# Optimization experiments

Measured on AMD Instinct MI355X. Metric: run time of the kernel, lower is better.

## Reference

```python
import jax, jax.numpy as jnp
import numpy as np

ODIM = 8192      # output dim (slice target)
MSIZE = 64       # tile size
N_BLOCKS = 1024  # size of shared block bank


def setup_inputs() -> dict:
    key = jax.random.key(0)
    k1, k2, k3, k4 = jax.random.split(key, 4)
    x = jax.random.normal(k1, (256, 8192), dtype=jnp.float32)
    # bank of msize x msize module blocks (scaled like fan-in init)
    blocks = jax.random.normal(k2, (N_BLOCKS, MSIZE, MSIZE), dtype=jnp.float32) * 0.02
    bound = 1.0 / np.sqrt(ODIM).astype(np.float32)
    bias = jax.random.uniform(k3, (ODIM,), dtype=jnp.float32, minval=-bound, maxval=bound)
    # parts: [icount, ocount] indices into the block bank
    parts = jax.random.randint(k4, (128, 128), 0, N_BLOCKS)
    return {"x": x, "blocks": blocks, "bias": bias, "parts": parts}


def reference(x, blocks, bias, parts):
    icount, ocount = parts.shape
    m = blocks.shape[-1]
    # build_mosaic: gather blocks per parts and tile into a dense weight matrix
    fc = blocks[parts]                                   # [ic, oc, m, m]
    fc_mat = fc.transpose(0, 2, 1, 3).reshape(icount * m, ocount * m)
    # idim (8192) is divisible by msize, so pad is identity (rem == 0 branch)
    y = x @ fc_mat                                       # [B, oc*m]
    y = y[..., :ODIM] + bias                             # slice + bias; post = Identity
    return y
```

## Files before the change

### kernel.cpp

```cpp
#include <hip/hip_runtime.h>
#include <stdint.h>

#define BATCH 256
#define IDIM  8192
#define ODIM  8192
#define MS    64
#define IC    128
#define OC    128
#define NB    1024

#define BM 256
#define BN 256
#define BK 64
#define KSPLIT 8
#define KT (IC / KSPLIT)

#define ABUF(s) ((s) * 16384)
#define BBUF(s) (32768 + (s) * 16384)

typedef __bf16 bf16x8 __attribute__((ext_vector_type(8)));
typedef float  floatx4 __attribute__((ext_vector_type(4)));

#define WAITCNT_VM(n) ((((n) & 15) | (((n) >> 4) << 14)) | 0x70 | 0xF00)

__device__ __forceinline__ void async_load16(unsigned short* lds_p, const unsigned short* g_p) {
    __builtin_amdgcn_global_load_lds(
        (const __attribute__((address_space(1))) unsigned int*)g_p,
        (__attribute__((address_space(3))) unsigned int*)lds_p,
        16, 0, 0);
}

__device__ __forceinline__ unsigned short f32_to_bf16(float f) {
    unsigned int u = __float_as_uint(f);
    u += 0x7FFFu + ((u >> 16) & 1u);
    return (unsigned short)(u >> 16);
}

#define XCONV_BLKS 1024
#define PT_BLKS 64
__global__ void k_convert(const float* __restrict__ x, const float* __restrict__ blocks,
                          const int* __restrict__ parts,
                          unsigned short* __restrict__ xb, unsigned short* __restrict__ bt,
                          int* __restrict__ pT) {
    __shared__ float tile[MS][MS + 1];
    int b = blockIdx.x;
    if (b < NB) {
        const float4* src4 = (const float4*)(blocks + (size_t)b * MS * MS);
        unsigned short* dst = bt + (size_t)b * MS * MS;
        #pragma unroll
        for (int i = 0; i < 4; ++i) {
            int slot = i * 256 + threadIdx.x;
            int r = slot >> 4, c4 = (slot & 15) * 4;
            float4 v = src4[slot];
            tile[r][c4 + 0] = v.x; tile[r][c4 + 1] = v.y;
            tile[r][c4 + 2] = v.z; tile[r][c4 + 3] = v.w;
        }
        __syncthreads();
        #pragma unroll
        for (int i = 0; i < 2; ++i) {
            int slot = i * 256 + threadIdx.x;
            int c = slot >> 3, o = slot & 7;
            union { unsigned short s[8]; uint4 v; } u;
            #pragma unroll
            for (int j = 0; j < 8; ++j) u.s[j] = f32_to_bf16(tile[o * 8 + j][c]);
            *(uint4*)(dst + c * MS + o * 8) = u.v;
        }
    } else if (b < NB + XCONV_BLKS) {
        int t = (b - NB) * 256 + threadIdx.x;
        const float4* x4 = (const float4*)x;
        float4 a = x4[2 * t], bb = x4[2 * t + 1];
        union { unsigned short s[8]; uint4 v; } u;
        u.s[0] = f32_to_bf16(a.x);  u.s[1] = f32_to_bf16(a.y);
        u.s[2] = f32_to_bf16(a.z);  u.s[3] = f32_to_bf16(a.w);
        u.s[4] = f32_to_bf16(bb.x); u.s[5] = f32_to_bf16(bb.y);
        u.s[6] = f32_to_bf16(bb.z); u.s[7] = f32_to_bf16(bb.w);
        ((uint4*)xb)[t] = u.v;
    } else {
        int t = (b - NB - XCONV_BLKS) * 256 + threadIdx.x;
        int oc = t >> 7, ic = t & 127;
        pT[t] = parts[ic * OC + oc];
    }
}

extern __shared__ unsigned short smem[];

__global__ __launch_bounds__(512, 2)
void k_mosaic_gemm(const unsigned short* __restrict__ xb,
                   const unsigned short* __restrict__ bt,
                   const int* __restrict__ pT,
                   float* __restrict__ partial) {
    const int tid  = threadIdx.x;
    const int lane = tid & 63;
    const int wave = tid >> 6;
    const int wrow = wave >> 2;
    const int wcol = wave & 3;
    const int ks = blockIdx.x;
    const int nt = blockIdx.y;

    const int ob0 = nt * 4;
    const int kb0 = ks * KT;

    const int row  = lane & 15;
    const int quad = lane >> 4;

    int pv = pT[(ob0 + quad) * IC + kb0 + row];

    const int swz0 = ((quad)     ^ (row & 7)) << 3;
    const int swz1 = ((quad + 4) ^ (row & 7)) << 3;
    const int a_b0 = (wrow * 128 + row) * MS + swz0;
    const int a_b1 = (wrow * 128 + row) * MS + swz1;
    const int b_b0 = (wcol * 64 + row) * MS + swz0;
    const int b_b1 = (wcol * 64 + row) * MS + swz1;

    floatx4 acc[8][4];
    #pragma unroll
    for (int mi = 0; mi < 8; ++mi)
        #pragma unroll
        for (int ni = 0; ni < 4; ++ni)
            acc[mi][ni] = (floatx4){0.f, 0.f, 0.f, 0.f};

    bf16x8 af[4], bfr[4];

#define STAGE_A(dstS, kb) do {                                                \
    _Pragma("unroll")                                                         \
    for (int j = 0; j < 4; ++j) {                                             \
        int slot = j * 512 + tid;               \
        int m = slot >> 3;                                                    \
        int oct = (slot & 7) ^ (m & 7);                                       \
        async_load16(smem + ABUF(dstS) + slot * 8,                            \
                     xb + (size_t)m * IDIM + (kb) * MS + oct * 8);            \
    } } while (0)

#define STAGE_B(dstS, tt) do {                                                \
    _Pragma("unroll")                                                         \
    for (int j = 0; j < 4; ++j) {                                             \
        int q = __shfl(pv, j * 16 + (tt));                                    \
        int slot = j * 512 + tid;                                             \
        int n = slot >> 3;                                                    \
        int oct = (slot & 7) ^ (n & 7);                                       \
        async_load16(smem + BBUF(dstS) + slot * 8,                            \
                     bt + (size_t)q * (MS * MS) + (n & 63) * MS + oct * 8);   \
    } } while (0)

#define LOAD_A(S, abase, mh) do {                                             \
    _Pragma("unroll")                                                         \
    for (int mi = 0; mi < 4; ++mi)                                            \
        af[mi] = *(const bf16x8*)(smem + ABUF(S) + (abase) + (mh) * 4096 + mi * 1024); \
    } while (0)

#define LOAD_B(S, bbase) do {                                                 \
    _Pragma("unroll")                                                         \
    for (int ni = 0; ni < 4; ++ni)                                            \
        bfr[ni] = *(const bf16x8*)(smem + BBUF(S) + (bbase) + ni * 1024);     \
    } while (0)

#define MFMA16(mh) do {                                                       \
    _Pragma("unroll")                                                         \
    for (int mi = 0; mi < 4; ++mi)                                            \
        _Pragma("unroll")                                                     \
        for (int ni = 0; ni < 4; ++ni)                                        \
            acc[(mh) * 4 + mi][ni] = __builtin_amdgcn_mfma_f32_16x16x32_bf16( \
                af[mi], bfr[ni], acc[(mh) * 4 + mi][ni], 0, 0, 0);            \
    } while (0)

#define COMPUTE(AS, BS) do {                                                  \
    LOAD_A(AS, a_b0, 0); LOAD_B(BS, b_b0); MFMA16(0);                         \
    LOAD_A(AS, a_b0, 1);                   MFMA16(1);                         \
    LOAD_A(AS, a_b1, 0); LOAD_B(BS, b_b1); MFMA16(0);                         \
    LOAD_A(AS, a_b1, 1);                   MFMA16(1);                         \
    } while (0)

#define TILE(t, AS, BS, AN, BN2, STA, STB, WN) do {                           \
    if (STA) STAGE_A(AN, kb0 + (t) + 1);                                      \
    if (STB) STAGE_B(BN2, (t) + 2);                                           \
    __builtin_amdgcn_sched_barrier(0);                                        \
    __builtin_amdgcn_s_waitcnt(WAITCNT_VM(WN));                               \
    __builtin_amdgcn_s_barrier();                                             \
    __builtin_amdgcn_sched_barrier(0);                                        \
    COMPUTE(AS, BS);                                                          \
    __builtin_amdgcn_sched_barrier(0);                                        \
    __builtin_amdgcn_s_barrier();                                             \
    __builtin_amdgcn_sched_barrier(0);                                        \
    } while (0)

    STAGE_A(0, kb0);
    STAGE_B(0, 0);
    STAGE_B(1, 1);

    #pragma unroll 1
    for (int t6 = 0; t6 < 12; t6 += 6) {
        TILE(t6 + 0, 0, 0, 1, 2, 1, 1, 12);
        TILE(t6 + 1, 1, 1, 0, 0, 1, 1, 12);
        TILE(t6 + 2, 0, 2, 1, 1, 1, 1, 12);
        TILE(t6 + 3, 1, 0, 0, 2, 1, 1, 12);
        TILE(t6 + 4, 0, 1, 1, 0, 1, 1, 12);
        TILE(t6 + 5, 1, 2, 0, 1, 1, 1, 12);
    }
    TILE(12, 0, 0, 1, 2, 1, 1, 12);
    TILE(13, 1, 1, 0, 0, 1, 1, 12);
    TILE(14, 0, 2, 1, 0, 1, 0, 8);
    TILE(15, 1, 0, 0, 0, 0, 0, 0);

    float* out = partial + (size_t)ks * ((size_t)BATCH * ODIM);
    #pragma unroll
    for (int mi8 = 0; mi8 < 8; ++mi8)
        #pragma unroll
        for (int ni = 0; ni < 4; ++ni)
            #pragma unroll
            for (int r = 0; r < 4; ++r) {
                int rowg = wrow * 128 + mi8 * 16 + quad * 4 + r;
                int colg = nt * BN + wcol * 64 + ni * 16 + row;
                out[(size_t)rowg * ODIM + colg] = acc[mi8][ni][r];
            }
}

__global__ void k_reduce_bias(const float* __restrict__ partial,
                              const float* __restrict__ bias,
                              float* __restrict__ out) {
    int t = blockIdx.x * 256 + threadIdx.x;
    const float4* b4 = (const float4*)bias;
    float4 c = b4[t & (ODIM / 4 - 1)];
    float4 r = {c.x, c.y, c.z, c.w};
    #pragma unroll
    for (int k = 0; k < KSPLIT; ++k) {
        const float4* p = (const float4*)(partial + (size_t)k * BATCH * ODIM);
        float4 a = p[t];
        r.x += a.x; r.y += a.y; r.z += a.z; r.w += a.w;
    }
    ((float4*)out)[t] = r;
}

extern "C" void kernel_launch(void* const* d_in, const int* in_sizes, int n_in,
                              void* d_out, int out_size, void* d_ws, size_t ws_size,
                              hipStream_t stream) {
    const float* x      = (const float*)d_in[0];
    const float* blocks = (const float*)d_in[1];
    const float* bias   = (const float*)d_in[2];
    const int*   parts  = (const int*)d_in[3];
    float* out = (float*)d_out;

    char* ws = (char*)d_ws;
    unsigned short* xb      = (unsigned short*)ws;
    unsigned short* btb     = (unsigned short*)(ws + (4u << 20));
    int*            pTr     = (int*)(ws + (12u << 20));
    float*          partial = (float*)(ws + (13u << 20));

    static bool attr_set = false;
    if (!attr_set) {
        hipFuncSetAttribute((const void*)k_mosaic_gemm,
                            hipFuncAttributeMaxDynamicSharedMemorySize, 160 * 1024);
        attr_set = true;
    }

    k_convert<<<NB + XCONV_BLKS + PT_BLKS, 256, 0, stream>>>(x, blocks, parts, xb, btb, pTr);
    k_mosaic_gemm<<<dim3(KSPLIT, ODIM / BN), 512, 160 * 1024, stream>>>(xb, btb, pTr, partial);
    k_reduce_bias<<<(BATCH * ODIM) / (256 * 4), 256, 0, stream>>>(partial, bias, out);
}
```

Baseline: 128.6 us.

## Load B fragments directly from global into registers, drop LDS staging for B

Rather than staging the gathered weight blocks into LDS with async copies, each wave now reads its B fragments straight from global memory into registers. The fragments are double-buffered in two register sets, with the load for the next k-half issued in the middle of the current tile's MFMAs. This removes the B LDS buffers, so the LDS request drops from 160KB to 64KB, and removes LDS read traffic for B. The cost is more global/L2 load latency exposed to the waves, less cross-wave reuse of B, and higher register pressure. The waitcnt counts were also changed, which may not match the new load counts.

Measured after the change: 135.9 us. 1.06x slower.

```diff
diff --git a/kernel.cpp b/kernel.cpp
--- a/kernel.cpp
+++ b/kernel.cpp
@@ -11,12 +11,10 @@
 
 #define BM 256
 #define BN 256
-#define BK 64
 #define KSPLIT 8
 #define KT (IC / KSPLIT)
 
 #define ABUF(s) ((s) * 16384)
-#define BBUF(s) (32768 + (s) * 16384)
 
 typedef __bf16 bf16x8 __attribute__((ext_vector_type(8)));
 typedef float  floatx4 __attribute__((ext_vector_type(4)));
@@ -109,8 +107,8 @@
     const int swz1 = ((quad + 4) ^ (row & 7)) << 3;
     const int a_b0 = (wrow * 128 + row) * MS + swz0;
     const int a_b1 = (wrow * 128 + row) * MS + swz1;
-    const int b_b0 = (wcol * 64 + row) * MS + swz0;
-    const int b_b1 = (wcol * 64 + row) * MS + swz1;
+
+    const int b_off = row * (MS * 2) + quad * 16;
 
     floatx4 acc[8][4];
     #pragma unroll
@@ -119,7 +117,8 @@
         for (int ni = 0; ni < 4; ++ni)
             acc[mi][ni] = (floatx4){0.f, 0.f, 0.f, 0.f};
 
-    bf16x8 af[4], bfr[4];
+    bf16x8 af[4];
+    bf16x8 bk0[4], bk1[4];
 
 #define STAGE_A(dstS, kb) do {                                                \
     _Pragma("unroll")                                                         \
@@ -131,16 +130,14 @@
                      xb + (size_t)m * IDIM + (kb) * MS + oct * 8);            \
     } } while (0)
 
-#define STAGE_B(dstS, tt) do {                                                \
-    _Pragma("unroll")                                                         \
-    for (int j = 0; j < 4; ++j) {                                             \
-        int q = __shfl(pv, j * 16 + (tt));                                    \
-        int slot = j * 512 + tid;                                             \
-        int n = slot >> 3;                                                    \
-        int oct = (slot & 7) ^ (n & 7);                                       \
-        async_load16(smem + BBUF(dstS) + slot * 8,                            \
-                     bt + (size_t)q * (MS * MS) + (n & 63) * MS + oct * 8);   \
-    } } while (0)
+#define LOADB(dstB, tt, kkh) do {                                             \
+    int q = __builtin_amdgcn_readfirstlane(__shfl(pv, wcol * 16 + (tt)));     \
+    const char* bq = (const char*)(bt + (size_t)q * (MS * MS)) + b_off        \
+                     + (kkh) * 64;                                            \
+    _Pragma("unroll")                                                         \
+    for (int ni = 0; ni < 4; ++ni)                                            \
+        dstB[ni] = *(const bf16x8*)(bq + ni * 2048);                          \
+    } while (0)
 
 #define LOAD_A(S, abase, mh) do {                                             \
     _Pragma("unroll")                                                         \
@@ -148,58 +145,44 @@
         af[mi] = *(const bf16x8*)(smem + ABUF(S) + (abase) + (mh) * 4096 + mi * 1024); \
     } while (0)
 
-#define LOAD_B(S, bbase) do {                                                 \
-    _Pragma("unroll")                                                         \
-    for (int ni = 0; ni < 4; ++ni)                                            \
-        bfr[ni] = *(const bf16x8*)(smem + BBUF(S) + (bbase) + ni * 1024);     \
-    } while (0)
-
-#define MFMA16(mh) do {                                                       \
+#define MFMA16(mh, BB) do {                                                   \
     _Pragma("unroll")                                                         \
     for (int mi = 0; mi < 4; ++mi)                                            \
         _Pragma("unroll")                                                     \
         for (int ni = 0; ni < 4; ++ni)                                        \
             acc[(mh) * 4 + mi][ni] = __builtin_amdgcn_mfma_f32_16x16x32_bf16( \
-                af[mi], bfr[ni], acc[(mh) * 4 + mi][ni], 0, 0, 0);            \
-    } while (0)
-
-#define COMPUTE(AS, BS) do {                                                  \
-    LOAD_A(AS, a_b0, 0); LOAD_B(BS, b_b0); MFMA16(0);                         \
-    LOAD_A(AS, a_b0, 1);                   MFMA16(1);                         \
-    LOAD_A(AS, a_b1, 0); LOAD_B(BS, b_b1); MFMA16(0);                         \
-    LOAD_A(AS, a_b1, 1);                   MFMA16(1);                         \
-    } while (0)
-
-#define TILE(t, AS, BS, AN, BN2, STA, STB, WN) do {                           \
+                af[mi], BB[ni], acc[(mh) * 4 + mi][ni], 0, 0, 0);             \
+    } while (0)
+
+#define TILE(t, AS, AN, STA, MIDB, WN) do {                                   \
     if (STA) STAGE_A(AN, kb0 + (t) + 1);                                      \
-    if (STB) STAGE_B(BN2, (t) + 2);                                           \
+    LOADB(bk1, (t), 1);                                                       \
     __builtin_amdgcn_sched_barrier(0);                                        \
     __builtin_amdgcn_s_waitcnt(WAITCNT_VM(WN));                               \
     __builtin_amdgcn_s_barrier();                                             \
     __builtin_amdgcn_sched_barrier(0);                                        \
-    COMPUTE(AS, BS);                                                          \
+    LOAD_A(AS, a_b0, 0); MFMA16(0, bk0);                                      \
+    LOAD_A(AS, a_b0, 1); MFMA16(1, bk0);                                      \
+    __builtin_amdgcn_sched_barrier(0);                                        \
+    if (MIDB) LOADB(bk0, (t) + 1, 0);                                         \
+    __builtin_amdgcn_sched_barrier(0);                                        \
+    LOAD_A(AS, a_b1, 0); MFMA16(0, bk1);                                      \
+    LOAD_A(AS, a_b1, 1); MFMA16(1, bk1);                                      \
     __builtin_amdgcn_sched_barrier(0);                                        \
     __builtin_amdgcn_s_barrier();                                             \
     __builtin_amdgcn_sched_barrier(0);                                        \
     } while (0)
 
     STAGE_A(0, kb0);
-    STAGE_B(0, 0);
-    STAGE_B(1, 1);
+    LOADB(bk0, 0, 0);
 
     #pragma unroll 1
-    for (int t6 = 0; t6 < 12; t6 += 6) {
-        TILE(t6 + 0, 0, 0, 1, 2, 1, 1, 12);
-        TILE(t6 + 1, 1, 1, 0, 0, 1, 1, 12);
-        TILE(t6 + 2, 0, 2, 1, 1, 1, 1, 12);
-        TILE(t6 + 3, 1, 0, 0, 2, 1, 1, 12);
-        TILE(t6 + 4, 0, 1, 1, 0, 1, 1, 12);
-        TILE(t6 + 5, 1, 2, 0, 1, 1, 1, 12);
-    }
-    TILE(12, 0, 0, 1, 2, 1, 1, 12);
-    TILE(13, 1, 1, 0, 0, 1, 1, 12);
-    TILE(14, 0, 2, 1, 0, 1, 0, 8);
-    TILE(15, 1, 0, 0, 0, 0, 0, 0);
+    for (int t2 = 0; t2 < 14; t2 += 2) {
+        TILE(t2,     0, 1, 1, 1, 12);
+        TILE(t2 + 1, 1, 0, 1, 1, 12);
+    }
+    TILE(14, 0, 1, 1, 1, 12);
+    TILE(15, 1, 0, 0, 0, 8);
 
     float* out = partial + (size_t)ks * ((size_t)BATCH * ODIM);
     #pragma unroll
@@ -248,11 +231,11 @@
     static bool attr_set = false;
     if (!attr_set) {
         hipFuncSetAttribute((const void*)k_mosaic_gemm,
-                            hipFuncAttributeMaxDynamicSharedMemorySize, 160 * 1024);
+                            hipFuncAttributeMaxDynamicSharedMemorySize, 64 * 1024);
         attr_set = true;
     }
 
     k_convert<<<NB + XCONV_BLKS + PT_BLKS, 256, 0, stream>>>(x, blocks, parts, xb, btb, pTr);
-    k_mosaic_gemm<<<dim3(KSPLIT, ODIM / BN), 512, 160 * 1024, stream>>>(xb, btb, pTr, partial);
+    k_mosaic_gemm<<<dim3(KSPLIT, ODIM / BN), 512, 64 * 1024, stream>>>(xb, btb, pTr, partial);
     k_reduce_bias<<<(BATCH * ODIM) / (256 * 4), 256, 0, stream>>>(partial, bias, out);
 }
```
